# Kernel tuning notes

Hardware: AMD Instinct MI355X
Metric: run time of the kernel (lower is better)

The kernel has to match this reference:

```python
import jax, jax.numpy as jnp
import numpy as np

N_NODES, N_EDGES, B, L = 20000, 320000, 64, 48
EMB, OUT, HEADS, HID = 256, 64, 4, 512
S_DIM, R_DIM = 64, 64
TIME_NUM, CAT_NUM = 48, 201


def lrelu(x, s=0.2):
    return jnp.where(x >= 0, x, s * x)


def gru_cell(x, h, Wi, Wh, bi, bh):
    # PyTorch GRUCell math
    gi = x @ Wi.T + bi
    gh = h @ Wh.T + bh
    ir, iz, ig = jnp.split(gi, 3, axis=-1)
    hr, hz, hg = jnp.split(gh, 3, axis=-1)
    r = jax.nn.sigmoid(ir + hr)
    z = jax.nn.sigmoid(iz + hz)
    n = jnp.tanh(ig + r * hg)
    return (1.0 - z) * n + z * h


def gru_seq(x, Wi, Wh, bi, bh, reverse=False):
    # x: [B,L,D] -> [B,L,H]
    xs = jnp.swapaxes(x, 0, 1)
    if reverse:
        xs = xs[::-1]
    h0 = jnp.zeros((x.shape[0], Wh.shape[1]), x.dtype)

    def step(h, xt):
        h2 = gru_cell(xt, h, Wi, Wh, bi, bh)
        return h2, h2

    _, ys = jax.lax.scan(step, h0, xs)
    if reverse:
        ys = ys[::-1]
    return jnp.swapaxes(ys, 0, 1)


def setup_inputs() -> dict:
    key = jax.random.key(0)
    ks = iter(jax.random.split(key, 64))
    f32 = jnp.float32

    def rn(shape, s=0.1):
        return (s * jax.random.normal(next(ks), shape)).astype(f32)

    inp = {
        'graph_x': jnp.arange(N_NODES),
        'edge_index': jax.random.randint(next(ks), (2, N_EDGES), 0, N_NODES),
        'edge_attr': jax.random.uniform(next(ks), (N_EDGES,), f32),
        'batch_x': jax.random.randint(next(ks), (B, L), 0, N_NODES),
        'batch_time': jax.random.randint(next(ks), (B, L), 0, TIME_NUM),
        'batch_cat': jax.random.randint(next(ks), (B, L), 0, CAT_NUM),
        'poi_time': jax.random.randint(next(ks), (N_NODES,), 0, TIME_NUM),
        'poi_cat': jax.random.randint(next(ks), (N_NODES,), 0, CAT_NUM),
        # params
        'node_emb': rn((N_NODES, EMB), 1.0),
        'W_gat': rn((EMB, HEADS * OUT), 0.05),
        'att_src': rn((HEADS, OUT), 0.05),
        'att_dst': rn((HEADS, OUT), 0.05),
        'gat_bias': rn((HEADS * OUT,)),
        'time_table': rn((TIME_NUM, EMB), 1.0),
        'cat_table': rn((CAT_NUM, EMB), 1.0),
        'W_w': rn((EMB, 3 * EMB)), 'b_w': rn((EMB,)),
        'Wi_f': rn((3 * HID, EMB), 0.05), 'Wh_f': rn((3 * HID, HID), 0.05),
        'bi_f': jnp.zeros((3 * HID,), f32), 'bh_f': jnp.zeros((3 * HID,), f32),
        'Wi_bw': rn((3 * HID, EMB), 0.05), 'Wh_bw': rn((3 * HID, HID), 0.05),
        'bi_bw': jnp.zeros((3 * HID,), f32), 'bh_bw': jnp.zeros((3 * HID,), f32),
        'Wi_u': rn((3 * HID, 2 * HID), 0.05), 'Wh_u': rn((3 * HID, HID), 0.05),
        'bi_u': jnp.zeros((3 * HID,), f32), 'bh_u': jnp.zeros((3 * HID,), f32),
        'Ws_m': rn((S_DIM, 2 * HID)), 'bs_m': rn((S_DIM,)),
        'Ws_lv': rn((S_DIM, 2 * HID)), 'bs_lv': rn((S_DIM,)),
        'Wr_m': rn((R_DIM, HID)), 'br_m': rn((R_DIM,)),
        'Wr_lv': rn((R_DIM, HID)), 'br_lv': rn((R_DIM,)),
        'Wp1_i': rn((3 * HID, R_DIM), 0.05), 'Wp1_h': rn((3 * HID, HID), 0.05),
        'bp1_i': jnp.zeros((3 * HID,), f32), 'bp1_h': jnp.zeros((3 * HID,), f32),
        'Wp2_i': rn((3 * HID, HID), 0.05), 'Wp2_h': rn((3 * HID, HID), 0.05),
        'bp2_i': jnp.zeros((3 * HID,), f32), 'bp2_h': jnp.zeros((3 * HID,), f32),
        'Wpm': rn((R_DIM, HID)), 'bpm': rn((R_DIM,)),
        'Wplv': rn((R_DIM, HID)), 'bplv': rn((R_DIM,)),
        'Wd': rn((N_NODES, S_DIM + R_DIM)), 'bd': rn((N_NODES,)),
    }
    return inp


def forward(graph_x, edge_index, edge_attr, batch_x, batch_time, batch_cat,
            poi_time, poi_cat, node_emb, W_gat, att_src, att_dst, gat_bias,
            time_table, cat_table, W_w, b_w, Wi_f, Wh_f, bi_f, bh_f,
            Wi_bw, Wh_bw, bi_bw, bh_bw, Wi_u, Wh_u, bi_u, bh_u,
            Ws_m, bs_m, Ws_lv, bs_lv, Wr_m, br_m, Wr_lv, br_lv,
            Wp1_i, Wp1_h, bp1_i, bp1_h, Wp2_i, Wp2_h, bp2_i, bp2_h,
            Wpm, bpm, Wplv, bplv, Wd, bd):
    Bn, Ln = batch_x.shape
    N = node_emb.shape[0]
    heads, C = att_src.shape

    # --- weighted GAT layer over the POI graph ---
    h = node_emb[graph_x]                                   # [N, EMB]
    xW = (h @ W_gat).reshape(N, heads, C)                   # [N, H, C]
    src, dst = edge_index[0], edge_index[1]
    e = lrelu((xW * att_src).sum(-1)[src] + (xW * att_dst).sum(-1)[dst])  # [E, H]
    emax = jax.ops.segment_max(e, dst, num_segments=N)
    a = jnp.exp(e - emax[dst])
    asum = jax.ops.segment_sum(a, dst, num_segments=N)
    att = a / (asum[dst] + 1e-16)
    msg = (att * edge_attr[:, None])[:, :, None] * xW[src]  # [E, H, C]
    p = jax.ops.segment_sum(msg, dst, num_segments=N).reshape(N, heads * C) + gat_bias

    # --- per-step feature build ---
    p_h = p[batch_x]                                        # [B, L, EMB]
    t_e = time_table[batch_time]
    c_e = cat_table[batch_cat]
    ph = jnp.concatenate([p_h, t_e, c_e], axis=2) @ W_w.T + b_w  # [B, L, EMB]

    # --- posterior encode: biGRU -> s, uniGRU -> r ---
    f_fwd = gru_seq(ph, Wi_f, Wh_f, bi_f, bh_f)
    f_bwd = gru_seq(ph, Wi_bw, Wh_bw, bi_bw, bh_bw, reverse=True)
    features = jnp.concatenate([f_fwd, f_bwd], axis=2)      # [B, L, 2H]
    Hh = Wh_f.shape[1]
    frontal = features[:, Ln - 1, :Hh]
    backward = features[:, 0, Hh:2 * Hh]
    g = jnp.concatenate([frontal, backward], axis=1)
    s_mean = lrelu(g @ Ws_m.T + bs_m)
    s_logvar = lrelu(g @ Ws_lv.T + bs_lv)

    key = jax.random.key(42)
    k1, k2, k3 = jax.random.split(key, 3)
    s_post = s_mean + jax.random.normal(k1, s_mean.shape, s_mean.dtype) * jnp.exp(0.5 * s_logvar)

    r_feat = gru_seq(features, Wi_u, Wh_u, bi_u, bh_u)      # [B, L, H]
    r_mean = r_feat @ Wr_m.T + br_m
    r_logvar = r_feat @ Wr_lv.T + br_lv
    r_post = r_mean + jax.random.normal(k2, r_mean.shape, r_mean.dtype) * jnp.exp(0.5 * r_logvar)

    # --- prior: 2-layer GRUCell unroll fed with shifted r_post ---
    Rd = r_post.shape[2]
    r_in = jnp.concatenate([jnp.zeros((Bn, 1, Rd), r_post.dtype), r_post[:, :-1]], axis=1)
    r_in_t = jnp.swapaxes(r_in, 0, 1)                       # [L, B, R]
    eps = jax.random.normal(k3, (Ln, Bn, Rd), r_post.dtype)

    def pstep(carry, xe):
        h1, h2 = carry
        rt, ep = xe
        h1 = gru_cell(rt, h1, Wp1_i, Wp1_h, bp1_i, bp1_h)
        h2 = gru_cell(h1, h2, Wp2_i, Wp2_h, bp2_i, bp2_h)
        mt = h2 @ Wpm.T + bpm
        lvt = h2 @ Wplv.T + bplv
        rp = mt + ep * jnp.exp(0.5 * lvt)
        return (h1, h2), (mt, lvt, rp)

    h10 = jnp.zeros((Bn, Hh), r_post.dtype)
    h20 = jnp.zeros((Bn, Hh), r_post.dtype)
    _, (ms, lvs, rps) = jax.lax.scan(pstep, (h10, h20), (r_in_t, eps))
    r_mean_prior = jnp.swapaxes(ms, 0, 1)
    r_logvar_prior = jnp.swapaxes(lvs, 0, 1)
    r_prior = jnp.swapaxes(rps, 0, 1)

    # --- decode ---
    s_expand = jnp.broadcast_to(s_post[:, None, :], (Bn, Ln, s_post.shape[1]))
    zf = jnp.concatenate([r_post, s_expand], axis=2)
    recon_x = zf @ Wd.T + bd                                # [B, L, node_num]
    return (s_mean, s_logvar, s_post, r_mean, r_logvar, r_post,
            r_mean_prior, r_logvar_prior, r_prior, recon_x)


def reference(graph_x, edge_index, edge_attr, batch_x, batch_time, batch_cat,
              poi_time, poi_cat, node_emb, W_gat, att_src, att_dst, gat_bias,
              time_table, cat_table, W_w, b_w, Wi_f, Wh_f, bi_f, bh_f,
              Wi_bw, Wh_bw, bi_bw, bh_bw, Wi_u, Wh_u, bi_u, bh_u,
              Ws_m, bs_m, Ws_lv, bs_lv, Wr_m, br_m, Wr_lv, br_lv,
              Wp1_i, Wp1_h, bp1_i, bp1_h, Wp2_i, Wp2_h, bp2_i, bp2_h,
              Wpm, bpm, Wplv, bplv, Wd, bd):
    return forward(graph_x, edge_index, edge_attr, batch_x, batch_time, batch_cat,
                   poi_time, poi_cat, node_emb, W_gat, att_src, att_dst, gat_bias,
                   time_table, cat_table, W_w, b_w, Wi_f, Wh_f, bi_f, bh_f,
                   Wi_bw, Wh_bw, bi_bw, bh_bw, Wi_u, Wh_u, bi_u, bh_u,
                   Ws_m, bs_m, Ws_lv, bs_lv, Wr_m, br_m, Wr_lv, br_lv,
                   Wp1_i, Wp1_h, bp1_i, bp1_h, Wp2_i, Wp2_h, bp2_i, bp2_h,
                   Wpm, bpm, Wplv, bplv, Wd, bd)
```

## Files before the change

kernel.cpp:

```cpp
#include <hip/hip_runtime.h>
#include <stdint.h>
#include <stddef.h>

#define DEV __device__ __forceinline__

typedef float f32x4 __attribute__((ext_vector_type(4)));

__host__ __device__ inline void tf2x32(uint32_t k0, uint32_t k1,
                                       uint32_t x0, uint32_t x1,
                                       uint32_t* o0, uint32_t* o1) {
  uint32_t ks2 = k0 ^ k1 ^ 0x1BD11BDAu;
  uint32_t ks[3] = {k0, k1, ks2};
  x0 += k0; x1 += k1;
  const uint32_t R[8] = {13u,15u,26u,6u,17u,29u,16u,24u};
  for (int r = 0; r < 5; ++r) {
    const uint32_t* rot = (r & 1) ? (R + 4) : R;
    for (int i = 0; i < 4; ++i) {
      x0 += x1;
      uint32_t d = rot[i];
      x1 = (x1 << d) | (x1 >> (32u - d));
      x1 ^= x0;
    }
    x0 += ks[(r + 1) % 3];
    x1 += ks[(r + 2) % 3] + (uint32_t)(r + 1);
  }
  *o0 = x0; *o1 = x1;
}

DEV float erfinv_approx(float x) {
  float w = -logf((1.0f - x) * (1.0f + x));
  float p;
  if (w < 5.0f) {
    w = w - 2.5f;
    p = 2.81022636e-08f;
    p = fmaf(p, w, 3.43273939e-07f);
    p = fmaf(p, w, -3.5233877e-06f);
    p = fmaf(p, w, -4.39150654e-06f);
    p = fmaf(p, w, 0.00021858087f);
    p = fmaf(p, w, -0.00125372503f);
    p = fmaf(p, w, -0.00417768164f);
    p = fmaf(p, w, 0.246640727f);
    p = fmaf(p, w, 1.50140941f);
  } else {
    w = sqrtf(w) - 3.0f;
    p = -0.000200214257f;
    p = fmaf(p, w, 0.000100950558f);
    p = fmaf(p, w, 0.00134934322f);
    p = fmaf(p, w, -0.00367342844f);
    p = fmaf(p, w, 0.00573950773f);
    p = fmaf(p, w, -0.0076224613f);
    p = fmaf(p, w, 0.00943887047f);
    p = fmaf(p, w, 1.00167406f);
    p = fmaf(p, w, 2.83297682f);
  }
  return p * x;
}

DEV float normal_part(uint32_t ka, uint32_t kb, uint32_t idx) {
  uint32_t b1, b2;
  tf2x32(ka, kb, 0u, idx, &b1, &b2);
  uint32_t bits = b1 ^ b2;
  float f = __uint_as_float((bits >> 9) | 0x3f800000u) - 1.0f;
  const float lo = -0.99999994f;
  float u = f * 2.0f + lo;
  u = fmaxf(lo, u);
  return 1.41421356f * erfinv_approx(u);
}

DEV float lrelu(float x) { return x >= 0.f ? x : 0.2f * x; }
DEV float sigm(float x) { return 1.0f / (1.0f + expf(-x)); }

DEV float gru_out(float ir, float iz, float ig, float hr, float hz, float hg, float hprev) {
  float r = sigm(ir + hr);
  float z = sigm(iz + hz);
  float n = tanhf(ig + r * hg);
  return (1.0f - z) * n + z * hprev;
}

DEV float dot4f(float4 a, float4 b, float acc) {
  return fmaf(a.x, b.x, fmaf(a.y, b.y, fmaf(a.z, b.z, fmaf(a.w, b.w, acc))));
}

template <int K4>
DEV void dot2(const float* __restrict__ h, const float* __restrict__ w0,
              const float* __restrict__ w1, float& a0, float& a1) {
  const float4* h4 = (const float4*)h;
  const float4* p0 = (const float4*)w0;
  const float4* p1 = (const float4*)w1;
  #pragma unroll 4
  for (int k = 0; k < K4; ++k) {
    float4 hv = h4[k];
    float4 v0 = p0[k], v1 = p1[k];
    a0 = dot4f(hv, v0, a0);
    a1 = dot4f(hv, v1, a1);
  }
}

template <int K4>
DEV void dotT3p(const float* __restrict__ hp, int b,
                const float* __restrict__ w0, const float* __restrict__ w1,
                const float* __restrict__ w2, float& a0, float& a1, float& a2) {
  const float4* __restrict__ w04 = (const float4*)w0;
  const float4* __restrict__ w14 = (const float4*)w1;
  const float4* __restrict__ w24 = (const float4*)w2;
  const float4* __restrict__ h4 = (const float4*)hp;
  #pragma unroll
  for (int k4 = 0; k4 < K4; ++k4) {
    float4 hv = h4[k4 * 64 + b];
    a0 = dot4f(w04[k4], hv, a0);
    a1 = dot4f(w14[k4], hv, a1);
    a2 = dot4f(w24[k4], hv, a2);
  }
}

template <int K4>
DEV void dotT3_lds(const float* __restrict__ hl, int b,
                   const float* __restrict__ w0, const float* __restrict__ w1,
                   const float* __restrict__ w2, float& a0, float& a1, float& a2) {
  const float4* __restrict__ h4 = (const float4*)hl;
  const float4* __restrict__ w04 = (const float4*)w0;
  const float4* __restrict__ w14 = (const float4*)w1;
  const float4* __restrict__ w24 = (const float4*)w2;
  #pragma unroll 8
  for (int k4 = 0; k4 < K4; ++k4) {
    float4 hv = h4[k4 * 64 + b];
    a0 = dot4f(w04[k4], hv, a0);
    a1 = dot4f(w14[k4], hv, a1);
    a2 = dot4f(w24[k4], hv, a2);
  }
}

template <int N16>
DEV void stage_lds(float* __restrict__ dst, const float* __restrict__ src) {
  const float4* __restrict__ s4 = (const float4*)src;
  float4* __restrict__ d4 = (float4*)dst;
  int tid = threadIdx.x;
  constexpr int CH = (N16 < 16) ? N16 : 16;
  #pragma unroll
  for (int r = 0; r < N16; r += CH) {
    float4 v[CH];
    #pragma unroll
    for (int u = 0; u < CH; ++u) v[u] = s4[(size_t)(r + u) * 256 + tid];
    #pragma unroll
    for (int u = 0; u < CH; ++u) d4[(size_t)(r + u) * 256 + tid] = v[u];
  }
}

DEV size_t pk(int k, int b) { return (size_t)(k >> 2) * 256 + b * 4 + (k & 3); }

DEV void coh_store_i(int* p, int v) {
  asm volatile("global_store_dword %0, %1, off sc0 sc1" :: "v"(p), "v"(v) : "memory");
}
DEV void coh_store_f(float* p, float v) {
  asm volatile("global_store_dword %0, %1, off sc0 sc1" :: "v"(p), "v"(v) : "memory");
}
DEV void coh_store_f4(float* p, f32x4 v) {
  asm volatile("global_store_dwordx4 %0, %1, off sc0 sc1" :: "v"(p), "v"(v) : "memory");
}
DEV int coh_load_i(const int* p) {
  int v;
  asm volatile("global_load_dword %0, %1, off sc0 sc1\n\ts_waitcnt vmcnt(0)"
               : "=v"(v) : "v"(p) : "memory");
  return v;
}

#define FSTRIDE 32

DEV void flag_barrier(int* __restrict__ flags, int nblk, int myidx, int gen) {
  asm volatile("s_waitcnt vmcnt(0)" ::: "memory");
  __syncthreads();
  if (threadIdx.x == 0) coh_store_i(flags + (size_t)myidx * FSTRIDE, gen);
  if ((int)threadIdx.x < nblk) {
    int spins = 0;
    while (coh_load_i(flags + (size_t)threadIdx.x * FSTRIDE) < gen) {
      __builtin_amdgcn_s_sleep(4);
      if (++spins > (1 << 21)) break;
    }
  }
  __syncthreads();
}

DEV void wait_group(const int* __restrict__ flags, int nblk, int thr) {
  if ((int)threadIdx.x < nblk) {
    int spins = 0;
    while (coh_load_i(flags + (size_t)threadIdx.x * FSTRIDE) < thr) {
      __builtin_amdgcn_s_sleep(4);
      if (++spins > (1 << 21)) break;
    }
  }
  __syncthreads();
}

DEV void store_packed_tile4(float* dst_t, const float (*smem)[64], int j0) {
  if (threadIdx.x < 64) {
    int bb = threadIdx.x;
    f32x4 v;
    v.x = smem[0][bb];
    v.y = smem[1][bb];
    v.z = smem[2][bb];
    v.w = smem[3][bb];
    coh_store_f4(dst_t + (size_t)(j0 >> 2) * 256 + bb * 4, v);
  }
}

#define GBM 128
#define GBN 128
#define GBK 16

__global__ __launch_bounds__(256) void gemm_nt(
    const float* __restrict__ A, const float* __restrict__ Bt,
    const float* __restrict__ bias, float* __restrict__ C,
    int M, int N, int K, const int* __restrict__ gatherA, int trGI) {
  __shared__ float As[GBK][GBM + 4];
  __shared__ float Bs[GBK][GBN + 4];
  const int bm = blockIdx.y * GBM;
  const int bn = blockIdx.x * GBN;
  const int tid = threadIdx.x;
  const int tx = tid & 15;
  const int ty = tid >> 4;
  float acc[8][8];
  #pragma unroll
  for (int i = 0; i < 8; ++i)
    #pragma unroll
    for (int j = 0; j < 8; ++j) acc[i][j] = 0.f;

  for (int k0 = 0; k0 < K; k0 += GBK) {
    #pragma unroll
    for (int s = 0; s < 2; ++s) {
      int f = tid + s * 256;
      int r = f >> 2, kq = f & 3;
      int row = bm + r;
      float4 v = make_float4(0.f, 0.f, 0.f, 0.f);
      if (row < M) {
        int ar = gatherA ? gatherA[row] : row;
        v = *(const float4*)&A[(size_t)ar * K + k0 + kq * 4];
      }
      As[kq * 4 + 0][r] = v.x;
      As[kq * 4 + 1][r] = v.y;
      As[kq * 4 + 2][r] = v.z;
      As[kq * 4 + 3][r] = v.w;
    }
    #pragma unroll
    for (int s = 0; s < 2; ++s) {
      int f = tid + s * 256;
      int r = f >> 2, kq = f & 3;
      int col = bn + r;
      float4 v = make_float4(0.f, 0.f, 0.f, 0.f);
      if (col < N) v = *(const float4*)&Bt[(size_t)col * K + k0 + kq * 4];
      Bs[kq * 4 + 0][r] = v.x;
      Bs[kq * 4 + 1][r] = v.y;
      Bs[kq * 4 + 2][r] = v.z;
      Bs[kq * 4 + 3][r] = v.w;
    }
    __syncthreads();
    #pragma unroll
    for (int kk = 0; kk < GBK; ++kk) {
      float4 a0 = *(const float4*)&As[kk][ty * 4];
      float4 a1 = *(const float4*)&As[kk][64 + ty * 4];
      float4 b0 = *(const float4*)&Bs[kk][tx * 4];
      float4 b1 = *(const float4*)&Bs[kk][64 + tx * 4];
      float av[8] = {a0.x, a0.y, a0.z, a0.w, a1.x, a1.y, a1.z, a1.w};
      float bv[8] = {b0.x, b0.y, b0.z, b0.w, b1.x, b1.y, b1.z, b1.w};
      #pragma unroll
      for (int i = 0; i < 8; ++i)
        #pragma unroll
        for (int j = 0; j < 8; ++j)
          acc[i][j] = fmaf(av[i], bv[j], acc[i][j]);
    }
    __syncthreads();
  }
  #pragma unroll
  for (int i = 0; i < 8; ++i) {
    int row = bm + ((i < 4) ? (ty * 4 + i) : (64 + ty * 4 + i - 4));
    if (row >= M) continue;
    if (trGI) {
      #pragma unroll
      for (int j = 0; j < 8; ++j) {
        int col = bn + ((j < 4) ? (tx * 4 + j) : (64 + tx * 4 + j - 4));
        if (col >= N) continue;
        float v = acc[i][j] + (bias ? bias[col] : 0.f);
        int bb = row / 48, tt = row - bb * 48;
        C[((size_t)tt * N + col) * 64 + bb] = v;
      }
    } else {
      #pragma unroll
      for (int g = 0; g < 2; ++g) {
        int col0 = bn + g * 64 + tx * 4;
        if (col0 + 3 >= N) continue;
        float4 v;
        v.x = acc[i][g * 4 + 0] + (bias ? bias[col0 + 0] : 0.f);
        v.y = acc[i][g * 4 + 1] + (bias ? bias[col0 + 1] : 0.f);
        v.z = acc[i][g * 4 + 2] + (bias ? bias[col0 + 2] : 0.f);
        v.w = acc[i][g * 4 + 3] + (bias ? bias[col0 + 3] : 0.f);
        *(float4*)&C[(size_t)row * N + col0] = v;
      }
    }
  }
}

__global__ void k_transpose(const float* __restrict__ W, float* __restrict__ Wt,
                            int rows, int cols) {
  int idx = blockIdx.x * 256 + threadIdx.x;
  if (idx >= rows * cols) return;
  int r = idx / cols, c = idx % cols;
  Wt[(size_t)c * rows + r] = W[idx];
}

__global__ void k_count_deg(const int* __restrict__ dst, int* __restrict__ deg, int nE) {
  int e = blockIdx.x * 256 + threadIdx.x;
  if (e < nE) atomicAdd(&deg[dst[e]], 1);
}

__global__ __launch_bounds__(1024) void k_scan(const int* __restrict__ deg,
                                               int* __restrict__ off,
                                               int* __restrict__ cursor, int n) {
  __shared__ int tmp[1024];
  __shared__ int carry_s;
  if (threadIdx.x == 0) carry_s = 0;
  __syncthreads();
  for (int base = 0; base < n; base += 1024) {
    int i = base + (int)threadIdx.x;
    int v = (i < n) ? deg[i] : 0;
    tmp[threadIdx.x] = v;
    __syncthreads();
    for (int s = 1; s < 1024; s <<= 1) {
      int t = (threadIdx.x >= (unsigned)s) ? tmp[threadIdx.x - s] : 0;
      __syncthreads();
      tmp[threadIdx.x] += t;
      __syncthreads();
    }
    int incl = tmp[threadIdx.x];
    int base_c = carry_s;
    int excl = incl - v;
    if (i < n) { off[i] = base_c + excl; cursor[i] = base_c + excl; }
    __syncthreads();
    if (threadIdx.x == 1023) carry_s = base_c + incl;
    __syncthreads();
  }
  if (threadIdx.x == 0) off[n] = carry_s;
}

__global__ void k_scatter(const int* __restrict__ dst, int* __restrict__ cursor,
                          int* __restrict__ csr, int nE) {
  int e = blockIdx.x * 256 + threadIdx.x;
  if (e < nE) {
    int pos = atomicAdd(&cursor[dst[e]], 1);
    csr[pos] = e;
  }
}

__global__ void k_alpha(const float* __restrict__ xW, const float* __restrict__ att_src,
                        const float* __restrict__ att_dst, float* __restrict__ as_,
                        float* __restrict__ ad_) {
  int i = blockIdx.x * 256 + threadIdx.x;
  if (i >= 80000) return;
  int n = i >> 2, h = i & 3;
  const float* xr = xW + (size_t)n * 256 + h * 64;
  const float* s = att_src + h * 64;
  const float* d = att_dst + h * 64;
  float a = 0.f, b = 0.f;
  dot2<16>(xr, s, d, a, b);
  as_[i] = a;
  ad_[i] = b;
}

__global__ __launch_bounds__(256) void k_gat_node(
    const float* __restrict__ xW, const float* __restrict__ as_,
    const float* __restrict__ ad_, const int* __restrict__ off,
    const int* __restrict__ csr, const int* __restrict__ esrc,
    const float* __restrict__ eattr, const float* __restrict__ gat_bias,
    float* __restrict__ p) {
  int n = blockIdx.x;
  int h = threadIdx.x >> 6;
  int c = threadIdx.x & 63;
  int s0 = off[n], s1 = off[n + 1];
  float adn = ad_[n * 4 + h];
  float m = -3.0e38f;
  for (int idx = s0; idx < s1; ++idx) {
    int e = csr[idx];
    int s = esrc[e];
    float ev = lrelu(as_[s * 4 + h] + adn);
    m = fmaxf(m, ev);
  }
  float sum = 0.f;
  for (int idx = s0; idx < s1; ++idx) {
    int e = csr[idx];
    int s = esrc[e];
    float ev = lrelu(as_[s * 4 + h] + adn);
    sum += expf(ev - m);
  }
  float acc = 0.f;
  for (int idx = s0; idx < s1; ++idx) {
    int e = csr[idx];
    int s = esrc[e];
    float ev = lrelu(as_[s * 4 + h] + adn);
    float w = expf(ev - m) / (sum + 1e-16f) * eattr[e];
    acc = fmaf(w, xW[(size_t)s * 256 + h * 64 + c], acc);
  }
  p[(size_t)n * 256 + h * 64 + c] = acc + gat_bias[h * 64 + c];
}

__global__ void k_build_X(const float* __restrict__ p, const float* __restrict__ tt,
                          const float* __restrict__ ct, const int* __restrict__ bx,
                          const int* __restrict__ btm, const int* __restrict__ bct,
                          float* __restrict__ X) {
  int idx = blockIdx.x * 256 + threadIdx.x;
  if (idx >= 3072 * 768) return;
  int rl = idx / 768, c = idx % 768;
  float v;
  if (c < 256) v = p[(size_t)bx[rl] * 256 + c];
  else if (c < 512) v = tt[(size_t)btm[rl] * 256 + (c - 256)];
  else v = ct[(size_t)bct[rl] * 256 + (c - 512)];
  X[idx] = v;
}

__global__ __launch_bounds__(256, 1) void k_gru_bidir_fused(
    const float* __restrict__ giT_f, const float* __restrict__ giT_b,
    const float* __restrict__ Wh_f, const float* __restrict__ bh_f,
    const float* __restrict__ Wh_b, const float* __restrict__ bh_b,
    float* __restrict__ features, float* __restrict__ hTb,
    int* __restrict__ flags) {
  __shared__ float lds_h[32768];
  __shared__ float smem[4][64];
  int w = threadIdx.x >> 6;
  int b = threadIdx.x & 63;
  int slot = blockIdx.x * 4 + w;
  int dir = slot >> 9;
  int j = slot & 511;
  int j0 = (blockIdx.x * 4) & 511;
  int gbid = blockIdx.x & 127;
  int* gflags = flags + (size_t)dir * 128 * FSTRIDE;
  const float* Wh = dir ? Wh_b : Wh_f;
  const float* bh = dir ? bh_b : bh_f;
  const float* gi = dir ? giT_b : giT_f;
  const float* w0 = Wh + (size_t)j * 512;
  const float* w1 = Wh + (size_t)(512 + j) * 512;
  const float* w2 = Wh + (size_t)(1024 + j) * 512;
  float bhr = bh[j], bhz = bh[512 + j], bhg = bh[1024 + j];
  float* hD = hTb + (size_t)dir * 48 * 32768;
  for (int s = 0; s < 48; ++s) {
    int t = dir ? (47 - s) : s;
    const float* gir = gi + (size_t)t * 98304;
    float giv0 = gir[j * 64 + b];
    float giv1 = gir[(512 + j) * 64 + b];
    float giv2 = gir[(1024 + j) * 64 + b];
    float hr = bhr, hz = bhz, hg = bhg, hprev = 0.f;
    if (s > 0) {
      int tp = dir ? (t + 1) : (t - 1);
      stage_lds<32>(lds_h, hD + (size_t)tp * 32768);
      __syncthreads();
      dotT3_lds<128>(lds_h, b, w0, w1, w2, hr, hz, hg);
      hprev = lds_h[pk(j, b)];
    }
    float hnew = gru_out(giv0, giv1, giv2, hr, hz, hg, hprev);
    smem[w][b] = hnew;
    features[((size_t)(b * 48 + t)) * 1024 + dir * 512 + j] = hnew;
    __syncthreads();
    store_packed_tile4(hD + (size_t)t * 32768, smem, j0);
    flag_barrier(gflags, 128, gbid, s + 1);
  }
}

__global__ __launch_bounds__(256, 1) void k_gru_u_fused(
    const float* __restrict__ giT, const float* __restrict__ Wh,
    const float* __restrict__ bh, float* __restrict__ r_feat,
    float* __restrict__ hU, int* __restrict__ flags) {
  __shared__ float lds_h[32768];
  __shared__ float smem[4][64];
  int w = threadIdx.x >> 6;
  int b = threadIdx.x & 63;
  int j = blockIdx.x * 4 + w;
  int j0 = blockIdx.x * 4;
  const float* w0 = Wh + (size_t)j * 512;
  const float* w1 = Wh + (size_t)(512 + j) * 512;
  const float* w2 = Wh + (size_t)(1024 + j) * 512;
  float bhr = bh[j], bhz = bh[512 + j], bhg = bh[1024 + j];
  for (int s = 0; s < 48; ++s) {
    const float* gir = giT + (size_t)s * 98304;
    float giv0 = gir[j * 64 + b];
    float giv1 = gir[(512 + j) * 64 + b];
    float giv2 = gir[(1024 + j) * 64 + b];
    float hr = bhr, hz = bhz, hg = bhg, hprev = 0.f;
    if (s > 0) {
      stage_lds<32>(lds_h, hU + (size_t)(s - 1) * 32768);
      __syncthreads();
      dotT3_lds<128>(lds_h, b, w0, w1, w2, hr, hz, hg);
      hprev = lds_h[pk(j, b)];
    }
    float hnew = gru_out(giv0, giv1, giv2, hr, hz, hg, hprev);
    smem[w][b] = hnew;
    r_feat[((size_t)(b * 48 + s)) * 512 + j] = hnew;
    __syncthreads();
    store_packed_tile4(hU + (size_t)s * 32768, smem, j0);
    flag_barrier(flags, 128, blockIdx.x, s + 1);
  }
}

__global__ __launch_bounds__(256, 1) void k_prior_fused(
    const float* __restrict__ r_post,
    const float* __restrict__ Wp1_i, const float* __restrict__ Wp1_h,
    const float* __restrict__ bp1_i, const float* __restrict__ bp1_h,
    const float* __restrict__ Wp2_i, const float* __restrict__ Wp2_h,
    const float* __restrict__ bp2_i, const float* __restrict__ bp2_h,
    float* __restrict__ h1S, float* __restrict__ h2S,
    float* __restrict__ rT, int* __restrict__ flags) {
  __shared__ float lds_h[32768];
  __shared__ float smem[4][64];
  int w = threadIdx.x >> 6;
  int b = threadIdx.x & 63;
  int cell = blockIdx.x >> 7;
  int gbid = blockIdx.x & 127;
  int slot = blockIdx.x * 4 + w;
  int j = slot & 511;
  int j0 = (blockIdx.x * 4) & 511;
  int* flagsA = flags;
  int* flagsB = flags + (size_t)128 * FSTRIDE;

  if (cell == 0) {
    int tid = gbid * 256 + threadIdx.x;
    for (int x = tid; x < 48 * 64 * 64; x += 32768) {
      int b0 = x & 63;
      int i0 = (x >> 6) & 63;
      int t0 = x >> 12;
      coh_store_f(rT + (size_t)t0 * 4096 + pk(i0, b0),
                  r_post[((size_t)(b0 * 48 + t0)) * 64 + i0]);
    }
    flag_barrier(flagsA, 128, gbid, 1);

    const float* wi0 = Wp1_i + (size_t)j * 64;
    const float* wi1 = Wp1_i + (size_t)(512 + j) * 64;
    const float* wi2 = Wp1_i + (size_t)(1024 + j) * 64;
    const float* wh0 = Wp1_h + (size_t)j * 512;
    const float* wh1 = Wp1_h + (size_t)(512 + j) * 512;
    const float* wh2 = Wp1_h + (size_t)(1024 + j) * 512;
    float bir = bp1_i[j], biz = bp1_i[512 + j], big = bp1_i[1024 + j];
    float bhr = bp1_h[j], bhz = bp1_h[512 + j], bhg = bp1_h[1024 + j];
    for (int k = 0; k < 48; ++k) {
      float ir = bir, iz = biz, ig = big;
      float hr = bhr, hz = bhz, hg = bhg, hprev = 0.f;
      if (k > 0) {
        stage_lds<32>(lds_h, h1S + (size_t)(k - 1) * 32768);
        dotT3p<16>(rT + (size_t)(k - 1) * 4096, b, wi0, wi1, wi2, ir, iz, ig);
        __syncthreads();
        dotT3_lds<128>(lds_h, b, wh0, wh1, wh2, hr, hz, hg);
        hprev = lds_h[pk(j, b)];
      }
      smem[w][b] = gru_out(ir, iz, ig, hr, hz, hg, hprev);
      __syncthreads();
      store_packed_tile4(h1S + (size_t)k * 32768, smem, j0);
      flag_barrier(flagsA, 128, gbid, k + 2);
    }
  } else {
    const float* wi0 = Wp2_i + (size_t)j * 512;
    const float* wi1 = Wp2_i + (size_t)(512 + j) * 512;
    const float* wi2 = Wp2_i + (size_t)(1024 + j) * 512;
    const float* wh0 = Wp2_h + (size_t)j * 512;
    const float* wh1 = Wp2_h + (size_t)(512 + j) * 512;
    const float* wh2 = Wp2_h + (size_t)(1024 + j) * 512;
    float bir = bp2_i[j], biz = bp2_i[512 + j], big = bp2_i[1024 + j];
    float bhr = bp2_h[j], bhz = bp2_h[512 + j], bhg = bp2_h[1024 + j];
    for (int t = 0; t < 48; ++t) {
      wait_group(flagsA, 128, t + 2);
      stage_lds<32>(lds_h, h1S + (size_t)t * 32768);
      __syncthreads();
      float ir = bir, iz = biz, ig = big;
      dotT3_lds<128>(lds_h, b, wi0, wi1, wi2, ir, iz, ig);
      float hr = bhr, hz = bhz, hg = bhg, hprev = 0.f;
      if (t > 0) {
        __syncthreads();
        stage_lds<32>(lds_h, h2S + (size_t)(t - 1) * 32768);
        __syncthreads();
        dotT3_lds<128>(lds_h, b, wh0, wh1, wh2, hr, hz, hg);
        hprev = lds_h[pk(j, b)];
      }
      smem[w][b] = gru_out(ir, iz, ig, hr, hz, hg, hprev);
      __syncthreads();
      store_packed_tile4(h2S + (size_t)t * 32768, smem, j0);
      flag_barrier(flagsB, 128, gbid, t + 1);
    }
  }
}

__global__ void k_s_head(const float* __restrict__ features,
                         const float* __restrict__ Ws_m, const float* __restrict__ bs_m,
                         const float* __restrict__ Ws_lv, const float* __restrict__ bs_lv,
                         float* __restrict__ out, uint32_t ka, uint32_t kb) {
  int idx = blockIdx.x * 256 + threadIdx.x;
  if (idx >= 4096) return;
  int i = idx & 63, b = idx >> 6;
  const float* fr = features + ((size_t)(b * 48 + 47)) * 1024;
  const float* bk = features + ((size_t)(b * 48 + 0)) * 1024 + 512;
  const float* wm = Ws_m + (size_t)i * 1024;
  const float* wl = Ws_lv + (size_t)i * 1024;
  float m = 0.f, lv = 0.f;
  dot2<128>(fr, wm, wl, m, lv);
  dot2<128>(bk, wm + 512, wl + 512, m, lv);
  m = lrelu(m + bs_m[i]);
  lv = lrelu(lv + bs_lv[i]);
  float nz = normal_part(ka, kb, (uint32_t)idx);
  out[idx] = m;
  out[4096 + idx] = lv;
  out[8192 + idx] = m + nz * expf(0.5f * lv);
}

__global__ void k_r_head(const float* __restrict__ r_feat,
                         const float* __restrict__ Wr_m, const float* __restrict__ br_m,
                         const float* __restrict__ Wr_lv, const float* __restrict__ br_lv,
                         float* __restrict__ out, uint32_t ka, uint32_t kb) {
  int idx = blockIdx.x * 256 + threadIdx.x;
  if (idx >= 196608) return;
  int i = idx & 63;
  int bt = idx >> 6;
  const float* f = r_feat + (size_t)bt * 512;
  float m = 0.f, lv = 0.f;
  dot2<128>(f, Wr_m + (size_t)i * 512, Wr_lv + (size_t)i * 512, m, lv);
  m += br_m[i];
  lv += br_lv[i];
  float nz = normal_part(ka, kb, (uint32_t)idx);
  out[12288 + idx] = m;
  out[208896 + idx] = lv;
  out[405504 + idx] = m + nz * expf(0.5f * lv);
}

__global__ void k_prior_out(const float* __restrict__ h2S,
                            const float* __restrict__ Wpm, const float* __restrict__ bpm,
                            const float* __restrict__ Wplv, const float* __restrict__ bplv,
                            float* __restrict__ out, uint32_t ka, uint32_t kb) {
  int idx = blockIdx.x * 256 + threadIdx.x;
  if (idx >= 196608) return;
  int i = idx & 63;
  int bt = idx >> 6;
  int b = bt & 63;
  int t = bt >> 6;
  const float4* h4 = (const float4*)(h2S + (size_t)t * 32768);
  const float4* wm4 = (const float4*)(Wpm + (size_t)i * 512);
  const float4* wl4 = (const float4*)(Wplv + (size_t)i * 512);
  float m = 0.f, lv = 0.f;
  #pragma unroll 8
  for (int k4 = 0; k4 < 128; ++k4) {
    float4 hv = h4[k4 * 64 + b];
    m = dot4f(wm4[k4], hv, m);
    lv = dot4f(wl4[k4], hv, lv);
  }
  m += bpm[i];
  lv += bplv[i];
  float ep = normal_part(ka, kb, (uint32_t)idx);
  float rp = m + ep * expf(0.5f * lv);
  size_t o = ((size_t)b * 48 + t) * 64 + i;
  out[602112 + o] = m;
  out[798720 + o] = lv;
  out[995328 + o] = rp;
}

__global__ void k_build_zf(const float* __restrict__ out, float* __restrict__ zf) {
  int idx = blockIdx.x * 256 + threadIdx.x;
  if (idx >= 3072 * 128) return;
  int row = idx >> 7, c = idx & 127;
  float v;
  if (c < 64) v = out[405504 + row * 64 + c];
  else v = out[8192 + (row / 48) * 64 + (c - 64)];
  zf[idx] = v;
}

extern "C" void kernel_launch(void* const* d_in, const int* in_sizes, int n_in,
                              void* d_out, int out_size, void* d_ws, size_t ws_size,
                              hipStream_t stream) {
  const int* graph_x = (const int*)d_in[0];
  const int* edge_index = (const int*)d_in[1];
  const float* edge_attr = (const float*)d_in[2];
  const int* batch_x = (const int*)d_in[3];
  const int* batch_time = (const int*)d_in[4];
  const int* batch_cat = (const int*)d_in[5];
  const float* node_emb = (const float*)d_in[8];
  const float* W_gat = (const float*)d_in[9];
  const float* att_src = (const float*)d_in[10];
  const float* att_dst = (const float*)d_in[11];
  const float* gat_bias = (const float*)d_in[12];
  const float* time_table = (const float*)d_in[13];
  const float* cat_table = (const float*)d_in[14];
  const float* W_w = (const float*)d_in[15];
  const float* b_w = (const float*)d_in[16];
  const float* Wi_f = (const float*)d_in[17];
  const float* Wh_f = (const float*)d_in[18];
  const float* bi_f = (const float*)d_in[19];
  const float* bh_f = (const float*)d_in[20];
  const float* Wi_bw = (const float*)d_in[21];
  const float* Wh_bw = (const float*)d_in[22];
  const float* bi_bw = (const float*)d_in[23];
  const float* bh_bw = (const float*)d_in[24];
  const float* Wi_u = (const float*)d_in[25];
  const float* Wh_u = (const float*)d_in[26];
  const float* bi_u = (const float*)d_in[27];
  const float* bh_u = (const float*)d_in[28];
  const float* Ws_m = (const float*)d_in[29];
  const float* bs_m = (const float*)d_in[30];
  const float* Ws_lv = (const float*)d_in[31];
  const float* bs_lv = (const float*)d_in[32];
  const float* Wr_m = (const float*)d_in[33];
  const float* br_m = (const float*)d_in[34];
  const float* Wr_lv = (const float*)d_in[35];
  const float* br_lv = (const float*)d_in[36];
  const float* Wp1_i = (const float*)d_in[37];
  const float* Wp1_h = (const float*)d_in[38];
  const float* bp1_i = (const float*)d_in[39];
  const float* bp1_h = (const float*)d_in[40];
  const float* Wp2_i = (const float*)d_in[41];
  const float* Wp2_h = (const float*)d_in[42];
  const float* bp2_i = (const float*)d_in[43];
  const float* bp2_h = (const float*)d_in[44];
  const float* Wpm = (const float*)d_in[45];
  const float* bpm = (const float*)d_in[46];
  const float* Wplv = (const float*)d_in[47];
  const float* bplv = (const float*)d_in[48];
  const float* Wd = (const float*)d_in[49];
  const float* bd = (const float*)d_in[50];
  float* out = (float*)d_out;

  uint32_t k1a, k1b, k2a, k2b, k3a, k3b;
  tf2x32(0u, 42u, 0u, 0u, &k1a, &k1b);
  tf2x32(0u, 42u, 0u, 1u, &k2a, &k2b);
  tf2x32(0u, 42u, 0u, 2u, &k3a, &k3b);

  float* ws = (float*)d_ws;
  size_t o = 0;
  auto alloc = [&](size_t n) { float* q = ws + o; o += n; return q; };
  float* R1 = alloc(5120000);
  float* R2 = alloc(5120000);
  float* R3 = alloc(4718592);
  float* R4 = alloc(786432);
  float* as_ = alloc(80000);
  float* ad_ = alloc(80000);
  float* Wgt = alloc(65536);
  int* deg = (int*)alloc(20000);
  int* off = (int*)alloc(20001);
  int* cursor = (int*)alloc(20000);
  int* csr = (int*)alloc(320000);
  float* rT = alloc(196608);
  int* flags = (int*)alloc(32768);

  float* xW = R1;
  float* features = R1;
  float* r_feat = R1 + 3145728;
  float* p = R2;
  float* giT_b = R2;
  float* hU = R2;
  float* X = R3;
  float* giT_f = R3;
  float* giT_u = R3;
  float* h1S = R3;
  float* h2S = R3 + 1572864;
  float* ph = R4;
  float* zf = R4;
  float* hTb = out + 1191936;

  const int* esrc = edge_index;
  const int* edst = edge_index + 320000;

  dim3 B(256);

  (void)hipMemsetAsync(deg, 0, 20000 * sizeof(int), stream);
  (void)hipMemsetAsync(flags, 0, 32768 * sizeof(int), stream);

  k_transpose<<<dim3(256), B, 0, stream>>>(W_gat, Wgt, 256, 256);
  k_count_deg<<<dim3(1250), B, 0, stream>>>(edst, deg, 320000);
  k_scan<<<dim3(1), dim3(1024), 0, stream>>>(deg, off, cursor, 20000);
  k_scatter<<<dim3(1250), B, 0, stream>>>(edst, cursor, csr, 320000);
  gemm_nt<<<dim3(2, 157), B, 0, stream>>>(node_emb, Wgt, nullptr, xW,
                                          20000, 256, 256, graph_x, 0);
  k_alpha<<<dim3(313), B, 0, stream>>>(xW, att_src, att_dst, as_, ad_);
  k_gat_node<<<dim3(20000), B, 0, stream>>>(xW, as_, ad_, off, csr, esrc,
                                            edge_attr, gat_bias, p);

  k_build_X<<<dim3(9216), B, 0, stream>>>(p, time_table, cat_table, batch_x,
                                          batch_time, batch_cat, X);
  gemm_nt<<<dim3(2, 24), B, 0, stream>>>(X, W_w, b_w, ph, 3072, 256, 768,
                                         nullptr, 0);

  gemm_nt<<<dim3(12, 24), B, 0, stream>>>(ph, Wi_f, bi_f, giT_f, 3072, 1536, 256,
                                          nullptr, 1);
  gemm_nt<<<dim3(12, 24), B, 0, stream>>>(ph, Wi_bw, bi_bw, giT_b, 3072, 1536, 256,
                                          nullptr, 1);
  k_gru_bidir_fused<<<dim3(256), B, 0, stream>>>(
      giT_f, giT_b, Wh_f, bh_f, Wh_bw, bh_bw, features, hTb, flags);

  k_s_head<<<dim3(16), B, 0, stream>>>(features, Ws_m, bs_m, Ws_lv, bs_lv,
                                       out, k1a, k1b);

  gemm_nt<<<dim3(12, 24), B, 0, stream>>>(features, Wi_u, bi_u, giT_u,
                                          3072, 1536, 1024, nullptr, 1);
  k_gru_u_fused<<<dim3(128), B, 0, stream>>>(giT_u, Wh_u, bh_u, r_feat,
                                             hU, flags + 256 * FSTRIDE);

  k_r_head<<<dim3(768), B, 0, stream>>>(r_feat, Wr_m, br_m, Wr_lv, br_lv,
                                        out, k2a, k2b);

  k_prior_fused<<<dim3(256), B, 0, stream>>>(
      out + 405504, Wp1_i, Wp1_h, bp1_i, bp1_h, Wp2_i, Wp2_h, bp2_i, bp2_h,
      h1S, h2S, rT, flags + 384 * FSTRIDE);
  k_prior_out<<<dim3(768), B, 0, stream>>>(h2S, Wpm, bpm, Wplv, bplv,
                                           out, k3a, k3b);

  k_build_zf<<<dim3(1536), B, 0, stream>>>(out, zf);
  gemm_nt<<<dim3(157, 24), B, 0, stream>>>(zf, Wd, bd, out + 1191936,
                                           3072, 20000, 128, nullptr, 0);
}
```

Measured before the change: 4.746 ms.

## Run decoder GEMM in bf16 on MFMA matrix cores

```diff
diff --git a/kernel.cpp b/kernel.cpp
--- a/kernel.cpp
+++ b/kernel.cpp
@@ -5,6 +5,7 @@
 #define DEV __device__ __forceinline__
 
 typedef float f32x4 __attribute__((ext_vector_type(4)));
+typedef short bf16x8 __attribute__((ext_vector_type(8)));
 
 __host__ __device__ inline void tf2x32(uint32_t k0, uint32_t k1,
                                        uint32_t x0, uint32_t x1,
@@ -294,6 +295,69 @@
         v.w = acc[i][g * 4 + 3] + (bias ? bias[col0 + 3] : 0.f);
         *(float4*)&C[(size_t)row * N + col0] = v;
       }
+    }
+  }
+}
+
+__global__ void k_f32_to_bf16(const float* __restrict__ src,
+                              unsigned short* __restrict__ dst, int n) {
+  int i = blockIdx.x * 256 + threadIdx.x;
+  if (i >= n) return;
+  uint32_t u = __float_as_uint(src[i]);
+  uint32_t r = (u + 0x7fffu + ((u >> 16) & 1u)) >> 16;
+  dst[i] = (unsigned short)r;
+}
+
+__global__ __launch_bounds__(256) void gemm_bf16_mfma(
+    const unsigned short* __restrict__ A16, const unsigned short* __restrict__ B16,
+    const float* __restrict__ bias, float* __restrict__ C,
+    int M, int N, int K) {
+  int bm = blockIdx.x * 128;
+  int bn = blockIdx.y * 128;
+  int wave = threadIdx.x >> 6;
+  int lane = threadIdx.x & 63;
+  int wm = (wave & 1) * 64;
+  int wn = (wave >> 1) * 64;
+  int l15 = lane & 15;
+  int kg = lane >> 4;
+  f32x4 acc[4][4];
+  #pragma unroll
+  for (int mi = 0; mi < 4; ++mi)
+    #pragma unroll
+    for (int ni = 0; ni < 4; ++ni)
+      acc[mi][ni] = (f32x4){0.f, 0.f, 0.f, 0.f};
+
+  for (int kk = 0; kk < K; kk += 32) {
+    bf16x8 afrag[4], bfrag[4];
+    #pragma unroll
+    for (int mi = 0; mi < 4; ++mi) {
+      int row = bm + wm + mi * 16 + l15;
+      afrag[mi] = *(const bf16x8*)&A16[(size_t)row * K + kk + kg * 8];
+    }
+    #pragma unroll
+    for (int ni = 0; ni < 4; ++ni) {
+      int col = bn + wn + ni * 16 + l15;
+      if (col >= N) col = N - 1;
+      bfrag[ni] = *(const bf16x8*)&B16[(size_t)col * K + kk + kg * 8];
+    }
+    #pragma unroll
+    for (int mi = 0; mi < 4; ++mi)
+      #pragma unroll
+      for (int ni = 0; ni < 4; ++ni)
+        acc[mi][ni] = __builtin_amdgcn_mfma_f32_16x16x32_bf16(
+            afrag[mi], bfrag[ni], acc[mi][ni], 0, 0, 0);
+  }
+  #pragma unroll
+  for (int mi = 0; mi < 4; ++mi) {
+    #pragma unroll
+    for (int ni = 0; ni < 4; ++ni) {
+      int col = bn + wn + ni * 16 + l15;
+      if (col >= N) continue;
+      int rowb = bm + wm + mi * 16 + kg * 4;
+      float bv = bias[col];
+      #pragma unroll
+      for (int r = 0; r < 4; ++r)
+        C[(size_t)(rowb + r) * N + col] = acc[mi][ni][r] + bv;
     }
   }
 }
@@ -751,6 +815,8 @@
   float* h2S = R3 + 1572864;
   float* ph = R4;
   float* zf = R4;
+  unsigned short* Wd16 = (unsigned short*)R2;
+  unsigned short* zf16 = (unsigned short*)(R4 + 458752);
   float* hTb = out + 1191936;
 
   const int* esrc = edge_index;
@@ -791,6 +857,8 @@
   k_gru_u_fused<<<dim3(128), B, 0, stream>>>(giT_u, Wh_u, bh_u, r_feat,
                                              hU, flags + 256 * FSTRIDE);
 
+  k_f32_to_bf16<<<dim3(10000), B, 0, stream>>>(Wd, Wd16, 20000 * 128);
+
   k_r_head<<<dim3(768), B, 0, stream>>>(r_feat, Wr_m, br_m, Wr_lv, br_lv,
                                         out, k2a, k2b);
 
@@ -801,6 +869,7 @@
                                            out, k3a, k3b);
 
   k_build_zf<<<dim3(1536), B, 0, stream>>>(out, zf);
-  gemm_nt<<<dim3(157, 24), B, 0, stream>>>(zf, Wd, bd, out + 1191936,
-                                           3072, 20000, 128, nullptr, 0);
-}
+  k_f32_to_bf16<<<dim3(1536), B, 0, stream>>>(zf, zf16, 3072 * 128);
+  gemm_bf16_mfma<<<dim3(24, 157), B, 0, stream>>>(zf16, Wd16, bd,
+                                                  out + 1191936, 3072, 20000, 128);
+}
```

Result: faster. 4.637 ms (-2.3%).
